# Kernel tuning notes

Measured on AMD Instinct MI355X. Metric: run time of the kernel, lower is better.

Reference implementation:

```python
import jax, jax.numpy as jnp
import numpy as np

V_MIN, V_MAX, ATOMS, GAMMA = -40.0, 80.0, 51, 0.9
BATCH = 524288


def setup_inputs() -> dict:
    key = jax.random.key(0)
    k1, k2, k3 = jax.random.split(key, 3)
    p = jax.random.uniform(k1, (BATCH, ATOMS), dtype=jnp.float32)
    prob_next = p / jnp.sum(p, axis=-1, keepdims=True)  # valid categorical dist
    r = jax.random.normal(k2, (BATCH, 1), dtype=jnp.float32) * 10.0
    done = (jax.random.uniform(k3, (BATCH, 1)) < 0.1).astype(jnp.float32)
    return {"prob_next": prob_next, "r": r, "done": done}


def reference(prob_next, r, done):
    # C51 categorical projection (DistributionalDQN.singleBatch target computation)
    B, A = prob_next.shape
    delta = (V_MAX - V_MIN) / float(A - 1)
    support = jnp.linspace(V_MIN, V_MAX, A, dtype=prob_next.dtype)  # [A]
    atom_next = jnpp_clip = jnp.clip(r + GAMMA * (1.0 - done) * support[None, :], V_MIN, V_MAX)  # [B,A]
    b = (atom_next - V_MIN) / delta
    l = jnp.floor(b)
    u = jnp.ceil(b)
    d_m_l = (u + (l == u).astype(b.dtype) - b) * prob_next
    d_m_u = (b - l) * prob_next
    # vectorized per-row index_add_: flatten rows with offsets and do one scatter-add
    offs = (jnp.arange(B, dtype=jnp.int32) * A)[:, None]  # [B,1]
    li = offs + l.astype(jnp.int32)
    ui = offs + u.astype(jnp.int32)
    flat = jnp.zeros(B * A, dtype=prob_next.dtype)
    flat = flat.at[li.ravel()].add(d_m_l.ravel())
    flat = flat.at[ui.ravel()].add(d_m_u.ravel())
    return flat.reshape(B, A)
```

## Files before the change

kernel.cpp:

```cpp
#include <hip/hip_runtime.h>
#include <stdint.h>


#define ATOMS 51
#define RPB   64
#define THREADS 64
#define TILE_FLOATS (RPB * ATOMS)
#define TILE_VECS   (TILE_FLOATS / 4)
#define VEC_ITERS   ((TILE_VECS + THREADS - 1) / THREADS)
#define GRID_MAX 2048

typedef float vfloat4 __attribute__((ext_vector_type(4)));

__device__ __forceinline__ void compute_row(float* sb, int t, float rr, float dn) {
    const float c = 0.9f * (1.0f - dn);
    const float base = fmaf(-16.66666667f, c, (rr + 40.0f) * (1.0f / 2.4f));
    const int ib = t * ATOMS;

    float p[ATOMS];
    #pragma unroll
    for (int j = 0; j < ATOMS; ++j) p[j] = sb[ib + j];

    {
        vfloat4* sv = reinterpret_cast<vfloat4*>(sb);
        const vfloat4 z = {0.f, 0.f, 0.f, 0.f};
        #pragma unroll
        for (int i = 0; i < VEC_ITERS; ++i) {
            const int v = i * THREADS + t;
            if (v < TILE_VECS) sv[v] = z;
        }
    }

    int   cur  = (int)floorf(fminf(fmaxf(base, 0.0f), 50.0f));
    float vcur = 0.0f, vnext = 0.0f;
    #pragma unroll
    for (int j = 0; j < ATOMS; ++j) {
        float b = fmaf(c, (float)j, base);
        b = fminf(fmaxf(b, 0.0f), 50.0f);
        const float lf = floorf(b);
        const float f  = b - lf;
        const int  li  = (int)lf;
        if (li > cur) {
            sb[ib + cur] = vcur;
            vcur = vnext; vnext = 0.0f; ++cur;
        }
        vcur  = fmaf(1.0f - f, p[j], vcur);
        vnext = fmaf(f,        p[j], vnext);
    }
    sb[ib + cur] = vcur;
    if (cur < ATOMS - 1) sb[ib + cur + 1] = vnext;
}

__global__ __launch_bounds__(THREADS) void c51_project(
    const float* __restrict__ prob,
    const float* __restrict__ rin,
    const float* __restrict__ done,
    float* __restrict__ out,
    int nrows)
{
    __shared__ __align__(16) float s_buf[TILE_FLOATS];
    const int t = threadIdx.x;
    const int G = gridDim.x;
    const int ntiles = nrows / RPB;
    const int tail_rows = nrows - ntiles * RPB;

    int tk = blockIdx.x;
    if (tk < ntiles) {
        vfloat4 stg[VEC_ITERS];
        {
            const vfloat4* gsrc = reinterpret_cast<const vfloat4*>(prob + (size_t)tk * TILE_FLOATS);
            #pragma unroll
            for (int i = 0; i < VEC_ITERS; ++i) {
                const int v = i * THREADS + t;
                stg[i] = (v < TILE_VECS) ? gsrc[v] : (vfloat4){0.f, 0.f, 0.f, 0.f};
            }
        }
        float rv = rin[(size_t)tk * RPB + t];
        float dv = done[(size_t)tk * RPB + t];

        for (; tk < ntiles; tk += G) {
            {
                vfloat4* sv = reinterpret_cast<vfloat4*>(s_buf);
                #pragma unroll
                for (int i = 0; i < VEC_ITERS; ++i) {
                    const int v = i * THREADS + t;
                    if (v < TILE_VECS) sv[v] = stg[i];
                }
            }

            const int nxt = tk + G;
            float rnx = 0.0f, dnx = 0.0f;
            if (nxt < ntiles) {
                const vfloat4* gsrc = reinterpret_cast<const vfloat4*>(prob + (size_t)nxt * TILE_FLOATS);
                #pragma unroll
                for (int i = 0; i < VEC_ITERS; ++i) {
                    const int v = i * THREADS + t;
                    if (v < TILE_VECS) stg[i] = gsrc[v];
                }
                rnx = rin[(size_t)nxt * RPB + t];
                dnx = done[(size_t)nxt * RPB + t];
            }
            __builtin_amdgcn_sched_barrier(0);

            compute_row(s_buf, t, rv, dv);

            {
                vfloat4* dst = reinterpret_cast<vfloat4*>(out + (size_t)tk * TILE_FLOATS);
                const vfloat4* sv = reinterpret_cast<const vfloat4*>(s_buf);
                #pragma unroll
                for (int i = 0; i < VEC_ITERS; ++i) {
                    const int v = i * THREADS + t;
                    if (v < TILE_VECS) __builtin_nontemporal_store(sv[v], &dst[v]);
                }
            }

            rv = rnx; dv = dnx;
        }
    }

    if (tail_rows > 0 && blockIdx.x == 0) {
        const long long row0 = (long long)ntiles * RPB;
        const int n_e = tail_rows * ATOMS;
        const float* gsrc = prob + (size_t)row0 * ATOMS;
        __syncthreads();
        for (int e = t; e < n_e; e += THREADS) s_buf[e] = gsrc[e];
        __syncthreads();
        if (t < tail_rows) compute_row(s_buf, t, rin[row0 + t], done[row0 + t]);
        __syncthreads();
        float* dst = out + (size_t)row0 * ATOMS;
        for (int e = t; e < n_e; e += THREADS) dst[e] = s_buf[e];
    }
}

extern "C" void kernel_launch(void* const* d_in, const int* in_sizes, int n_in,
                              void* d_out, int out_size, void* d_ws, size_t ws_size,
                              hipStream_t stream) {
    const float* prob = (const float*)d_in[0];
    const float* r    = (const float*)d_in[1];
    const float* done = (const float*)d_in[2];
    float* outp = (float*)d_out;
    const int B = in_sizes[1];
    const int ntiles = B / RPB;
    int grid = ntiles < GRID_MAX ? ntiles : GRID_MAX;
    if (grid < 1) grid = 1;
    c51_project<<<dim3(grid), dim3(THREADS), 0, stream>>>(prob, r, done, outp, B);
}
```

Before: 40.37 us.

## Double-buffer register staging to prefetch two tiles ahead

New measurement: 40.56 us. No clear change (+0.5%).

```diff
diff --git a/kernel.cpp b/kernel.cpp
--- a/kernel.cpp
+++ b/kernel.cpp
@@ -11,6 +11,36 @@
 #define GRID_MAX 2048
 
 typedef float vfloat4 __attribute__((ext_vector_type(4)));
+
+__device__ __forceinline__ void load_tile(const float* __restrict__ prob,
+                                          int tile, int t, vfloat4* stg) {
+    const vfloat4* gsrc = reinterpret_cast<const vfloat4*>(prob + (size_t)tile * TILE_FLOATS);
+    #pragma unroll
+    for (int i = 0; i < VEC_ITERS; ++i) {
+        const int v = i * THREADS + t;
+        if (v < TILE_VECS) stg[i] = gsrc[v];
+    }
+}
+
+__device__ __forceinline__ void handoff_tile(float* sb, int t, const vfloat4* stg) {
+    vfloat4* sv = reinterpret_cast<vfloat4*>(sb);
+    #pragma unroll
+    for (int i = 0; i < VEC_ITERS; ++i) {
+        const int v = i * THREADS + t;
+        if (v < TILE_VECS) sv[v] = stg[i];
+    }
+}
+
+__device__ __forceinline__ void writeout_tile(float* __restrict__ out,
+                                              int tile, int t, const float* sb) {
+    vfloat4* dst = reinterpret_cast<vfloat4*>(out + (size_t)tile * TILE_FLOATS);
+    const vfloat4* sv = reinterpret_cast<const vfloat4*>(sb);
+    #pragma unroll
+    for (int i = 0; i < VEC_ITERS; ++i) {
+        const int v = i * THREADS + t;
+        if (v < TILE_VECS) __builtin_nontemporal_store(sv[v], &dst[v]);
+    }
+}
 
 __device__ __forceinline__ void compute_row(float* sb, int t, float rr, float dn) {
     const float c = 0.9f * (1.0f - dn);
@@ -66,55 +96,48 @@
 
     int tk = blockIdx.x;
     if (tk < ntiles) {
-        vfloat4 stg[VEC_ITERS];
-        {
-            const vfloat4* gsrc = reinterpret_cast<const vfloat4*>(prob + (size_t)tk * TILE_FLOATS);
-            #pragma unroll
-            for (int i = 0; i < VEC_ITERS; ++i) {
-                const int v = i * THREADS + t;
-                stg[i] = (v < TILE_VECS) ? gsrc[v] : (vfloat4){0.f, 0.f, 0.f, 0.f};
+        vfloat4 stgA[VEC_ITERS], stgB[VEC_ITERS];
+        float rA = 0.f, dA = 0.f, rB = 0.f, dB = 0.f;
+
+        load_tile(prob, tk, t, stgA);
+        rA = rin[(size_t)tk * RPB + t];
+        dA = done[(size_t)tk * RPB + t];
+        if (tk + G < ntiles) {
+            load_tile(prob, tk + G, t, stgB);
+            rB = rin[(size_t)(tk + G) * RPB + t];
+            dB = done[(size_t)(tk + G) * RPB + t];
+        }
+
+        for (; tk < ntiles; tk += 2 * G) {
+            {
+                handoff_tile(s_buf, t, stgA);
+                const int pf = tk + 2 * G;
+                float rnx = 0.f, dnx = 0.f;
+                if (pf < ntiles) {
+                    load_tile(prob, pf, t, stgA);
+                    rnx = rin[(size_t)pf * RPB + t];
+                    dnx = done[(size_t)pf * RPB + t];
+                }
+                __builtin_amdgcn_sched_barrier(0);
+                compute_row(s_buf, t, rA, dA);
+                writeout_tile(out, tk, t, s_buf);
+                rA = rnx; dA = dnx;
             }
-        }
-        float rv = rin[(size_t)tk * RPB + t];
-        float dv = done[(size_t)tk * RPB + t];
-
-        for (; tk < ntiles; tk += G) {
-            {
-                vfloat4* sv = reinterpret_cast<vfloat4*>(s_buf);
-                #pragma unroll
-                for (int i = 0; i < VEC_ITERS; ++i) {
-                    const int v = i * THREADS + t;
-                    if (v < TILE_VECS) sv[v] = stg[i];
+            const int tkB = tk + G;
+            if (tkB < ntiles) {
+                handoff_tile(s_buf, t, stgB);
+                const int pf = tkB + 2 * G;
+                float rnx = 0.f, dnx = 0.f;
+                if (pf < ntiles) {
+                    load_tile(prob, pf, t, stgB);
+                    rnx = rin[(size_t)pf * RPB + t];
+                    dnx = done[(size_t)pf * RPB + t];
                 }
+                __builtin_amdgcn_sched_barrier(0);
+                compute_row(s_buf, t, rB, dB);
+                writeout_tile(out, tkB, t, s_buf);
+                rB = rnx; dB = dnx;
             }
-
-            const int nxt = tk + G;
-            float rnx = 0.0f, dnx = 0.0f;
-            if (nxt < ntiles) {
-                const vfloat4* gsrc = reinterpret_cast<const vfloat4*>(prob + (size_t)nxt * TILE_FLOATS);
-                #pragma unroll
-                for (int i = 0; i < VEC_ITERS; ++i) {
-                    const int v = i * THREADS + t;
-                    if (v < TILE_VECS) stg[i] = gsrc[v];
-                }
-                rnx = rin[(size_t)nxt * RPB + t];
-                dnx = done[(size_t)nxt * RPB + t];
-            }
-            __builtin_amdgcn_sched_barrier(0);
-
-            compute_row(s_buf, t, rv, dv);
-
-            {
-                vfloat4* dst = reinterpret_cast<vfloat4*>(out + (size_t)tk * TILE_FLOATS);
-                const vfloat4* sv = reinterpret_cast<const vfloat4*>(s_buf);
-                #pragma unroll
-                for (int i = 0; i < VEC_ITERS; ++i) {
-                    const int v = i * THREADS + t;
-                    if (v < TILE_VECS) __builtin_nontemporal_store(sv[v], &dst[v]);
-                }
-            }
-
-            rv = rnx; dv = dnx;
         }
     }
 
```
